# Kernel tuning notes

Hardware: AMD Instinct MI355X
Metric: run time of the kernel (lower is better)

The kernel has to match this reference:

```python
import jax, jax.numpy as jnp
import numpy as np

CODEBOOK_SIZE = 8192
EMBED_DIM = 256


def setup_inputs() -> dict:
    key = jax.random.key(0)
    k_rep, k_cb = jax.random.split(key)
    rep = jax.random.normal(k_rep, (32, 2048, EMBED_DIM), dtype=jnp.float32)
    codebook = jax.random.normal(k_cb, (CODEBOOK_SIZE, EMBED_DIM), dtype=jnp.float32)
    return {"rep": rep, "codebook": codebook}


def reference(rep, codebook):
    # rep: [B, M, D], codebook: [K, D]
    B, M, D = rep.shape
    rep_flat = rep.reshape(-1, D)                                # [B*M, D]
    a2 = jnp.sum(rep_flat * rep_flat, axis=1, keepdims=True)     # [B*M, 1]
    b2 = jnp.sum(codebook * codebook, axis=1)[None, :]           # [1, K]
    ab = rep_flat @ codebook.T                                   # [B*M, K]
    dist = a2 + b2 - 2.0 * ab                                    # [B*M, K]
    idx = jnp.argmin(dist, axis=1).reshape(B, M)                 # [B, M] int
    return idx
```

## Files before the change

### kernel.cpp

```cpp
#include <hip/hip_runtime.h>
#include <stdint.h>

#define KCODES 8192
#define DIM 256
#define BN 128
#define NKT (KCODES / BN)
#define NSTEP (NKT * 4)

typedef _Float16 h16;
typedef __attribute__((ext_vector_type(8))) _Float16 f16x8;
typedef __attribute__((ext_vector_type(4))) float f32x4;

__device__ __forceinline__ void split8(const float* __restrict__ x, f16x8& h, f16x8& l) {
    #pragma unroll
    for (int i = 0; i < 8; ++i) {
        float v = x[i];
        _Float16 hv = (_Float16)v;
        h[i] = hv;
        l[i] = (_Float16)(v - (float)hv);
    }
}

__device__ __forceinline__ unsigned int ford(float f) {
    unsigned int b = __float_as_uint(f);
    return (b & 0x80000000u) ? ~b : (b | 0x80000000u);
}

#define WS_C2H   0u
#define WS_LC    32768u
#define WS_CN    65536u
#define WS_CNT   98304u
#define WS_LIST  98560u
#define WS_CAND  360704u
#define WS_THR   622848u
#define WS_KEYS  917504u
#define WS_BPH   2097152u

__global__ __launch_bounds__(256) void prep_kernel(const float* __restrict__ cb,
                                                   h16* __restrict__ Bp,
                                                   float* __restrict__ c2h,
                                                   float* __restrict__ lc,
                                                   float* __restrict__ cn) {
    const int tid = blockIdx.x * 256 + threadIdx.x;
    const int code = tid >> 5;
    const int grp = tid & 31;
    float x[8];
    *(float4*)&x[0] = *(const float4*)(cb + (size_t)code * DIM + grp * 8);
    *(float4*)&x[4] = *(const float4*)(cb + (size_t)code * DIM + grp * 8 + 4);
    f16x8 hh;
    float s = 0.f, sr = 0.f;
    #pragma unroll
    for (int i = 0; i < 8; ++i) {
        float v = x[i];
        _Float16 hv = (_Float16)v;
        hh[i] = hv;
        s += v * v;
        float rho = v - (float)hv;
        sr += rho * rho;
    }
    const int kt = code >> 7, c = code & 127;
    const int h = c >> 6, cl = c & 63;
    const int n = cl >> 4, c15 = cl & 15;
    const int cp = grp >> 3, j = (grp >> 2) & 1, g = grp & 3;
    const int lane = g * 16 + c15;
    const size_t off = (((size_t)((kt * 4 + cp) * 2 + h) * 8) + (n * 2 + j)) * 512 + lane * 8;
    *(f16x8*)(Bp + off) = hh;

    #pragma unroll
    for (int o = 16; o > 0; o >>= 1) { s += __shfl_xor(s, o); sr += __shfl_xor(sr, o); }
    if (grp == 0) {
        c2h[code] = 0.5f * s;
        cn[code] = sqrtf(s);
        lc[code] = sqrtf(sr);
    }
}

__global__ __launch_bounds__(256) void vq_pass1(
    const float* __restrict__ rep, const h16* __restrict__ Bp,
    const float* __restrict__ c2h, const float* __restrict__ lcA,
    const float* __restrict__ cnA, int* __restrict__ cand,
    float* __restrict__ thr) {

    __shared__ __align__(16) h16 lds[4][2][8][512];

    const int t = threadIdx.x;
    const int lane = t & 63;
    const int c15 = lane & 15;
    const int g = lane >> 4;
    const int w = t >> 6;
    const int rh = w >> 1;
    const int h = w & 1;
    const int brow = blockIdx.x * 64;

    f16x8 ah[2][8];
    float hnr[2][4], rnr[2][4];
    #pragma unroll
    for (int m = 0; m < 2; ++m) {
        const float* ar = rep + (size_t)(brow + rh * 32 + m * 16 + c15) * DIM + g * 8;
        float hs = 0.f, rs = 0.f;
        #pragma unroll
        for (int ch = 0; ch < 8; ++ch) {
            float x[8];
            *(float4*)&x[0] = *(const float4*)(ar + ch * 32);
            *(float4*)&x[4] = *(const float4*)(ar + ch * 32 + 4);
            #pragma unroll
            for (int i = 0; i < 8; ++i) {
                _Float16 hv = (_Float16)x[i];
                ah[m][ch][i] = hv;
                float hf = (float)hv;
                hs += hf * hf;
                float rho = x[i] - hf;
                rs += rho * rho;
            }
        }
        hs += __shfl_xor(hs, 16); hs += __shfl_xor(hs, 32);
        rs += __shfl_xor(rs, 16); rs += __shfl_xor(rs, 32);
        float hn = sqrtf(hs), rn = sqrtf(rs);
        #pragma unroll
        for (int r = 0; r < 4; ++r) {
            hnr[m][r] = __shfl(hn, g * 4 + r);
            rnr[m][r] = __shfl(rn, g * 4 + r);
        }
    }

    f32x4 acc[2][4];
    float u1v[2][4], u2v[2][4], Dl[4], Dc[4], D2[4];
    int u1i[2][4];
    #pragma unroll
    for (int m = 0; m < 2; ++m)
        #pragma unroll
        for (int n = 0; n < 4; ++n) {
            #pragma unroll
            for (int r = 0; r < 4; ++r) acc[m][n][r] = 0.f;
            u1v[m][n] = -3.4e38f; u2v[m][n] = -3.4e38f; u1i[m][n] = 0;
        }

    auto issueStep = [&](int S, int buf) {
        const h16* src = Bp + ((size_t)(S * 2 + h) * 8) * 512 + lane * 8;
        #pragma unroll
        for (int f = 0; f < 8; ++f)
            __builtin_amdgcn_global_load_lds(
                (const __attribute__((address_space(1))) uint32_t*)(src + f * 512),
                (__attribute__((address_space(3))) uint32_t*)(&lds[w][buf][f][lane * 8]),
                16, 0, 0);
    };

    asm volatile("s_waitcnt vmcnt(0)" ::: "memory");
    issueStep(0, 0);

    #pragma unroll 1
    for (int kt = 0; kt < NKT; ++kt) {
        const int ktbase = kt * BN;
        #pragma unroll
        for (int cp = 0; cp < 4; ++cp) {
            const int S = kt * 4 + cp;
            const int cur = cp & 1;
            if (cp == 0) {
                #pragma unroll
                for (int n = 0; n < 4; ++n) {
                    const int col = ktbase + h * 64 + n * 16 + c15;
                    Dl[n] = lcA[col];
                    Dc[n] = cnA[col];
                    D2[n] = 0.012f - c2h[col];
                }
            }
            if (S + 1 < NSTEP) issueStep(S + 1, cur ^ 1);
            if (S == NSTEP - 1) asm volatile("s_waitcnt vmcnt(0)" ::: "memory");
            else                asm volatile("s_waitcnt vmcnt(8)" ::: "memory");
            __builtin_amdgcn_sched_barrier(0);

            #pragma unroll
            for (int j = 0; j < 2; ++j) {
                const int ch = cp * 2 + j;
                #pragma unroll
                for (int n = 0; n < 4; ++n) {
                    f16x8 bh = *(const f16x8*)&lds[w][cur][n * 2 + j][lane * 8];
                    #pragma unroll
                    for (int m = 0; m < 2; ++m)
                        acc[m][n] = __builtin_amdgcn_mfma_f32_16x16x32_f16(ah[m][ch], bh, acc[m][n], 0, 0, 0);
                }
            }

            if (cp == 3) {
                #pragma unroll
                for (int n = 0; n < 4; ++n) {
                    const int col = ktbase + h * 64 + n * 16 + c15;
                    #pragma unroll
                    for (int m = 0; m < 2; ++m)
                        #pragma unroll
                        for (int r = 0; r < 4; ++r) {
                            float u = fmaf(hnr[m][r], Dl[n],
                                      fmaf(rnr[m][r], Dc[n], acc[m][n][r] + D2[n]));
                            if (u > u1v[m][r]) { u2v[m][r] = u1v[m][r]; u1v[m][r] = u; u1i[m][r] = col; }
                            else if (u > u2v[m][r]) u2v[m][r] = u;
                            acc[m][n][r] = 0.f;
                        }
                }
            }
        }
    }

    __syncthreads();
    float* sv1 = (float*)&lds[0][0][0][0];
    int* si1 = (int*)((char*)&lds[0][0][0][0] + 1024);
    float* sv2 = (float*)((char*)&lds[0][0][0][0] + 2048);
    #pragma unroll
    for (int m = 0; m < 2; ++m)
        #pragma unroll
        for (int r = 0; r < 4; ++r) {
            float a1 = u1v[m][r], a2 = u2v[m][r];
            int a1i = u1i[m][r];
            #pragma unroll
            for (int mask = 1; mask <= 8; mask <<= 1) {
                float b1 = __shfl_xor(a1, mask);
                int b1i = __shfl_xor(a1i, mask);
                float b2 = __shfl_xor(a2, mask);
                if (b1 > a1) { a2 = fmaxf(a1, b2); a1 = b1; a1i = b1i; }
                else         { a2 = fmaxf(b1, a2); }
            }
            if (c15 == 0) {
                const int rl = rh * 32 + m * 16 + g * 4 + r;
                sv1[rl * 2 + h] = a1;
                si1[rl * 2 + h] = a1i;
                sv2[rl * 2 + h] = a2;
            }
        }
    __syncthreads();
    if (t < 64) {
        float a1 = sv1[t * 2], a2 = sv2[t * 2];
        int a1i = si1[t * 2];
        float b1 = sv1[t * 2 + 1], b2 = sv2[t * 2 + 1];
        int b1i = si1[t * 2 + 1];
        float u1, u2; int u1idx;
        if (b1 > a1) { u1 = b1; u1idx = b1i; u2 = fmaxf(a1, b2); }
        else         { u1 = a1; u1idx = a1i; u2 = fmaxf(b1, a2); }
        cand[brow + t] = u1idx;
        thr[brow + t] = u2;
    }
}

__global__ __launch_bounds__(256) void resolve_kernel(
    const float* __restrict__ rep, const float* __restrict__ cb,
    const float* __restrict__ c2h, const int* __restrict__ cand,
    const float* __restrict__ thr, int* __restrict__ out,
    int* __restrict__ cnt, int* __restrict__ list, int N) {
    const int W = (blockIdx.x * 256 + threadIdx.x) >> 6;
    const int lane = threadIdx.x & 63;
    if (W >= N) return;
    const int ci = cand[W];
    const float4 rv = *(const float4*)(rep + (size_t)W * DIM + lane * 4);
    const float4 cv = *(const float4*)(cb + (size_t)ci * DIM + lane * 4);
    float p = rv.x * cv.x + rv.y * cv.y + rv.z * cv.z + rv.w * cv.w;
    #pragma unroll
    for (int off = 32; off > 0; off >>= 1) p += __shfl_down(p, off);
    if (lane == 0) {
        float sex = p - c2h[ci];
        out[W] = ci;
        if (!(sex > thr[W])) {
            int pos = atomicAdd(cnt, 1);
            list[pos] = W;
        }
    }
}

__global__ __launch_bounds__(256) void rescan_kernel(
    const float* __restrict__ rep, const float* __restrict__ cb,
    const float* __restrict__ c2h, const int* __restrict__ cnt_p,
    const int* __restrict__ list, unsigned long long* __restrict__ keys) {

    const int cnt = *cnt_p;
    const int base = blockIdx.x * 64;
    if (base >= cnt) return;
    const int nrows = min(64, cnt - base);
    const int ktbase = (int)blockIdx.y * BN;

    __shared__ __align__(16) h16 lds[2][BN * 64];
    const int t = threadIdx.x;
    const int lane = t & 63;
    const int w = t >> 6;
    const int c15 = lane & 15;
    const int g = lane >> 4;
    const int wrow = w * 16;

    const int aslot = wrow + c15;
    const int grow = list[base + (aslot < nrows ? aslot : 0)];
    f16x8 ah[8], al[8];
    {
        const float* ar = rep + (size_t)grow * DIM + g * 8;
        #pragma unroll
        for (int ch = 0; ch < 8; ++ch) {
            float x[8];
            *(float4*)&x[0] = *(const float4*)(ar + ch * 32);
            *(float4*)&x[4] = *(const float4*)(ar + ch * 32 + 4);
            split8(x, ah[ch], al[ch]);
        }
    }
    f32x4 acc[8];
    float cc[8];
    #pragma unroll
    for (int n = 0; n < 8; ++n) {
        #pragma unroll
        for (int r = 0; r < 4; ++r) acc[n][r] = 0.f;
        cc[n] = c2h[ktbase + n * 16 + c15];
    }

    const int scol = t >> 1;
    const int dslot = t & 1;
    float breg[16];
    auto loadB = [&](int ch) {
        const float* src = cb + (size_t)(ktbase + scol) * DIM + ch * 32 + dslot * 16;
        #pragma unroll
        for (int i = 0; i < 4; ++i) *(float4*)&breg[i * 4] = *(const float4*)(src + i * 4);
    };
    auto writeB = [&](int buf) {
        #pragma unroll
        for (int half = 0; half < 2; ++half) {
            f16x8 hh, ll;
            split8(&breg[half * 8], hh, ll);
            const int s = dslot * 2 + half;
            *(f16x8*)&lds[buf][scol * 64 + ((s ^ (scol & 7)) << 3)] = hh;
            *(f16x8*)&lds[buf][scol * 64 + (((s + 4) ^ (scol & 7)) << 3)] = ll;
        }
    };

    loadB(0);
    writeB(0);
    loadB(1);
    __syncthreads();

    #pragma unroll
    for (int chunk = 0; chunk < 8; ++chunk) {
        const int buf = chunk & 1;
        if (chunk != 7) writeB(buf ^ 1);
        if (chunk <= 5) loadB(chunk + 2);
        #pragma unroll
        for (int n = 0; n < 8; ++n) {
            const int bb = (n * 16 + c15) * 64;
            f16x8 bh = *(const f16x8*)&lds[buf][bb + ((g ^ (lane & 7)) << 3)];
            f16x8 bl = *(const f16x8*)&lds[buf][bb + (((4 + g) ^ (lane & 7)) << 3)];
            acc[n] = __builtin_amdgcn_mfma_f32_16x16x32_f16(ah[chunk], bh, acc[n], 0, 0, 0);
            acc[n] = __builtin_amdgcn_mfma_f32_16x16x32_f16(ah[chunk], bl, acc[n], 0, 0, 0);
            acc[n] = __builtin_amdgcn_mfma_f32_16x16x32_f16(al[chunk], bh, acc[n], 0, 0, 0);
            acc[n] = __builtin_amdgcn_mfma_f32_16x16x32_f16(al[chunk], bl, acc[n], 0, 0, 0);
        }
        __syncthreads();
    }

    #pragma unroll
    for (int r = 0; r < 4; ++r) {
        float bv = -3.4e38f;
        int bi = 0;
        #pragma unroll
        for (int n = 0; n < 8; ++n) {
            float s2 = acc[n][r] - cc[n];
            const int col = ktbase + n * 16 + c15;
            if (s2 > bv) { bv = s2; bi = col; }
        }
        #pragma unroll
        for (int mask = 1; mask <= 8; mask <<= 1) {
            float ov = __shfl_xor(bv, mask);
            int oi = __shfl_xor(bi, mask);
            if (ov > bv || (ov == bv && oi < bi)) { bv = ov; bi = oi; }
        }
        const int oslot = wrow + g * 4 + r;
        if (c15 == 0 && oslot < nrows) {
            unsigned long long key =
                ((unsigned long long)ford(bv) << 32) | (unsigned int)(~(unsigned int)bi);
            atomicMax(&keys[list[base + oslot]], key);
        }
    }
}

__global__ __launch_bounds__(256) void writeback_kernel(
    const int* __restrict__ cnt_p, const int* __restrict__ list,
    const unsigned long long* __restrict__ keys, int* __restrict__ out) {
    int i = blockIdx.x * 256 + threadIdx.x;
    if (i >= *cnt_p) return;
    int row = list[i];
    out[row] = (int)(~(unsigned int)(keys[row] & 0xFFFFFFFFull));
}

extern "C" void kernel_launch(void* const* d_in, const int* in_sizes, int n_in,
                              void* d_out, int out_size, void* d_ws, size_t ws_size,
                              hipStream_t stream) {
    const float* rep = (const float*)d_in[0];
    const float* cb = (const float*)d_in[1];
    const int N = in_sizes[0] / DIM;
    const int K = in_sizes[1] / DIM;
    (void)K;
    char* ws = (char*)d_ws;
    float* c2h = (float*)(ws + WS_C2H);
    float* lc  = (float*)(ws + WS_LC);
    float* cn  = (float*)(ws + WS_CN);
    int* cnt   = (int*)(ws + WS_CNT);
    int* list  = (int*)(ws + WS_LIST);
    int* cand  = (int*)(ws + WS_CAND);
    float* thr = (float*)(ws + WS_THR);
    unsigned long long* keys = (unsigned long long*)(ws + WS_KEYS);
    h16* Bph   = (h16*)(ws + WS_BPH);
    int* out = (int*)d_out;

    hipMemsetAsync(ws + WS_CNT, 0, 64, stream);
    hipMemsetAsync(keys, 0, (size_t)N * sizeof(unsigned long long), stream);
    prep_kernel<<<dim3(KCODES * 32 / 256), dim3(256), 0, stream>>>(cb, Bph, c2h, lc, cn);
    vq_pass1<<<dim3(N / 64), dim3(256), 0, stream>>>(rep, Bph, c2h, lc, cn, cand, thr);
    resolve_kernel<<<dim3(N / 4), dim3(256), 0, stream>>>(rep, cb, c2h, cand, thr, out, cnt, list, N);
    rescan_kernel<<<dim3(N / 64, NKT), dim3(256), 0, stream>>>(rep, cb, c2h, cnt, list, keys);
    writeback_kernel<<<dim3(N / 256), dim3(256), 0, stream>>>(cnt, list, keys, out);
}
```

Baseline: 522.9 us.

## Halve pass-1 code tile and use three-slot LDS ring with register prefetch

```diff
diff --git a/kernel.cpp b/kernel.cpp
--- a/kernel.cpp
+++ b/kernel.cpp
@@ -5,7 +5,8 @@
 #define DIM 256
 #define BN 128
 #define NKT (KCODES / BN)
-#define NSTEP (NKT * 4)
+#define NKT2 (KCODES / 64)
+#define NSTEP (NKT2 * 4)
 
 typedef _Float16 h16;
 typedef __attribute__((ext_vector_type(8))) _Float16 f16x8;
@@ -58,12 +59,12 @@
         float rho = v - (float)hv;
         sr += rho * rho;
     }
-    const int kt = code >> 7, c = code & 127;
-    const int h = c >> 6, cl = c & 63;
-    const int n = cl >> 4, c15 = cl & 15;
+    const int kt = code >> 6, cc = code & 63;
+    const int h = cc >> 5, c32 = cc & 31;
+    const int n = c32 >> 4, c15 = c32 & 15;
     const int cp = grp >> 3, j = (grp >> 2) & 1, g = grp & 3;
     const int lane = g * 16 + c15;
-    const size_t off = (((size_t)((kt * 4 + cp) * 2 + h) * 8) + (n * 2 + j)) * 512 + lane * 8;
+    const size_t off = ((size_t)((kt * 4 + cp) * 2 + h) * 4 + (n * 2 + j)) * 512 + lane * 8;
     *(f16x8*)(Bp + off) = hh;
 
     #pragma unroll
@@ -81,7 +82,7 @@
     const float* __restrict__ cnA, int* __restrict__ cand,
     float* __restrict__ thr) {
 
-    __shared__ __align__(16) h16 lds[4][2][8][512];
+    __shared__ __align__(16) h16 ring[4][3][2048];
 
     const int t = threadIdx.x;
     const int lane = t & 63;
@@ -123,68 +124,81 @@
         }
     }
 
-    f32x4 acc[2][4];
-    float u1v[2][4], u2v[2][4], Dl[4], Dc[4], D2[4];
+    f32x4 acc[2][2];
+    f16x8 bb[2][2][2];
+    float u1v[2][4], u2v[2][4], Dl[2], Dc[2], D2[2];
     int u1i[2][4];
     #pragma unroll
-    for (int m = 0; m < 2; ++m)
-        #pragma unroll
-        for (int n = 0; n < 4; ++n) {
+    for (int m = 0; m < 2; ++m) {
+        #pragma unroll
+        for (int n = 0; n < 2; ++n)
             #pragma unroll
             for (int r = 0; r < 4; ++r) acc[m][n][r] = 0.f;
-            u1v[m][n] = -3.4e38f; u2v[m][n] = -3.4e38f; u1i[m][n] = 0;
-        }
-
-    auto issueStep = [&](int S, int buf) {
-        const h16* src = Bp + ((size_t)(S * 2 + h) * 8) * 512 + lane * 8;
-        #pragma unroll
-        for (int f = 0; f < 8; ++f)
+        #pragma unroll
+        for (int r = 0; r < 4; ++r) { u1v[m][r] = -3.4e38f; u2v[m][r] = -3.4e38f; u1i[m][r] = 0; }
+    }
+
+    auto issueStep = [&](int S, int slot) {
+        const h16* src = Bp + (size_t)(S * 2 + h) * 2048 + lane * 8;
+        #pragma unroll
+        for (int f = 0; f < 4; ++f)
             __builtin_amdgcn_global_load_lds(
                 (const __attribute__((address_space(1))) uint32_t*)(src + f * 512),
-                (__attribute__((address_space(3))) uint32_t*)(&lds[w][buf][f][lane * 8]),
+                (__attribute__((address_space(3))) uint32_t*)(&ring[w][slot][f * 512 + lane * 8]),
                 16, 0, 0);
     };
 
     asm volatile("s_waitcnt vmcnt(0)" ::: "memory");
     issueStep(0, 0);
-
+    asm volatile("s_waitcnt vmcnt(0)" ::: "memory");
+    #pragma unroll
+    for (int f = 0; f < 4; ++f)
+        bb[0][f & 1][f >> 1] = *(const f16x8*)&ring[w][0][f * 512 + lane * 8];
+    issueStep(1, 1);
+
+    int s1 = 1, s2 = 2;
     #pragma unroll 1
-    for (int kt = 0; kt < NKT; ++kt) {
-        const int ktbase = kt * BN;
+    for (int kt = 0; kt < NKT2; ++kt) {
+        const int ktbase = kt * 64;
         #pragma unroll
         for (int cp = 0; cp < 4; ++cp) {
             const int S = kt * 4 + cp;
-            const int cur = cp & 1;
+            const int p = cp & 1;
             if (cp == 0) {
                 #pragma unroll
-                for (int n = 0; n < 4; ++n) {
-                    const int col = ktbase + h * 64 + n * 16 + c15;
+                for (int n = 0; n < 2; ++n) {
+                    const int col = ktbase + h * 32 + n * 16 + c15;
                     Dl[n] = lcA[col];
                     Dc[n] = cnA[col];
                     D2[n] = 0.012f - c2h[col];
                 }
             }
-            if (S + 1 < NSTEP) issueStep(S + 1, cur ^ 1);
-            if (S == NSTEP - 1) asm volatile("s_waitcnt vmcnt(0)" ::: "memory");
-            else                asm volatile("s_waitcnt vmcnt(8)" ::: "memory");
+            if (S + 2 < NSTEP) issueStep(S + 2, s2);
+            if (S < NSTEP - 2) asm volatile("s_waitcnt vmcnt(4)" ::: "memory");
+            else               asm volatile("s_waitcnt vmcnt(0)" ::: "memory");
             __builtin_amdgcn_sched_barrier(0);
+
+            if (S + 1 < NSTEP) {
+                const h16* nx = &ring[w][s1][0];
+                #pragma unroll
+                for (int f = 0; f < 4; ++f)
+                    bb[p ^ 1][f & 1][f >> 1] = *(const f16x8*)&nx[f * 512 + lane * 8];
+            }
 
             #pragma unroll
             for (int j = 0; j < 2; ++j) {
                 const int ch = cp * 2 + j;
                 #pragma unroll
-                for (int n = 0; n < 4; ++n) {
-                    f16x8 bh = *(const f16x8*)&lds[w][cur][n * 2 + j][lane * 8];
+                for (int n = 0; n < 2; ++n)
                     #pragma unroll
                     for (int m = 0; m < 2; ++m)
-                        acc[m][n] = __builtin_amdgcn_mfma_f32_16x16x32_f16(ah[m][ch], bh, acc[m][n], 0, 0, 0);
-                }
+                        acc[m][n] = __builtin_amdgcn_mfma_f32_16x16x32_f16(ah[m][ch], bb[p][j][n], acc[m][n], 0, 0, 0);
             }
 
             if (cp == 3) {
                 #pragma unroll
-                for (int n = 0; n < 4; ++n) {
-                    const int col = ktbase + h * 64 + n * 16 + c15;
+                for (int n = 0; n < 2; ++n) {
+                    const int col = ktbase + h * 32 + n * 16 + c15;
                     #pragma unroll
                     for (int m = 0; m < 2; ++m)
                         #pragma unroll
@@ -197,13 +211,15 @@
                         }
                 }
             }
+            s1 = (s1 + 1 == 3) ? 0 : s1 + 1;
+            s2 = (s2 + 1 == 3) ? 0 : s2 + 1;
         }
     }
 
     __syncthreads();
-    float* sv1 = (float*)&lds[0][0][0][0];
-    int* si1 = (int*)((char*)&lds[0][0][0][0] + 1024);
-    float* sv2 = (float*)((char*)&lds[0][0][0][0] + 2048);
+    float* sv1 = (float*)&ring[0][0][0];
+    int* si1 = (int*)((char*)&ring[0][0][0] + 1024);
+    float* sv2 = (float*)((char*)&ring[0][0][0] + 2048);
     #pragma unroll
     for (int m = 0; m < 2; ++m)
         #pragma unroll
@@ -335,9 +351,9 @@
         if (chunk <= 5) loadB(chunk + 2);
         #pragma unroll
         for (int n = 0; n < 8; ++n) {
-            const int bb = (n * 16 + c15) * 64;
-            f16x8 bh = *(const f16x8*)&lds[buf][bb + ((g ^ (lane & 7)) << 3)];
-            f16x8 bl = *(const f16x8*)&lds[buf][bb + (((4 + g) ^ (lane & 7)) << 3)];
+            const int bb2 = (n * 16 + c15) * 64;
+            f16x8 bh = *(const f16x8*)&lds[buf][bb2 + ((g ^ (lane & 7)) << 3)];
+            f16x8 bl = *(const f16x8*)&lds[buf][bb2 + (((4 + g) ^ (lane & 7)) << 3)];
             acc[n] = __builtin_amdgcn_mfma_f32_16x16x32_f16(ah[chunk], bh, acc[n], 0, 0, 0);
             acc[n] = __builtin_amdgcn_mfma_f32_16x16x32_f16(ah[chunk], bl, acc[n], 0, 0, 0);
             acc[n] = __builtin_amdgcn_mfma_f32_16x16x32_f16(al[chunk], bh, acc[n], 0, 0, 0);
```

Measured after the change: 586.0 us. +12.1%, slower.
